# Optimization experiments

Measured on AMD Instinct MI355X. Metric: run time of the kernel, lower is better.

The kernel has to match this reference:

```python
import jax, jax.numpy as jnp
import numpy as np
from jax import lax

B, T, D, H, O = 64, 2048, 512, 512, 512


def setup_inputs() -> dict:
    key = jax.random.key(0)
    ks = jax.random.split(key, 8)
    s_in = 1.0 / np.sqrt(D)
    s_h = 1.0 / np.sqrt(H)
    s_o = 1.0 / np.sqrt(O)
    return {
        "embeddings": jax.random.normal(ks[0], (B, T, D), dtype=jnp.float32),
        "last_logits": jax.random.normal(ks[1], (B, O), dtype=jnp.float32),
        "Whx": jax.random.normal(ks[2], (H, D), dtype=jnp.float32) * s_in,
        "bhx": jax.random.normal(ks[3], (H,), dtype=jnp.float32) * s_in,
        "Wyh": jax.random.normal(ks[4], (H, O), dtype=jnp.float32) * s_o,
        "byh": jax.random.normal(ks[5], (H,), dtype=jnp.float32) * s_o,
        "Wout": jax.random.normal(ks[6], (O, H), dtype=jnp.float32) * s_h,
        "bout": jax.random.normal(ks[7], (O,), dtype=jnp.float32) * s_h,
    }


def reference(embeddings, last_logits, Whx, bhx, Wyh, byh, Wout, bout):
    # Precompute the input projection for all timesteps in one big GEMM:
    # xh[b,t,h] = hx(x_t)  (time-parallel part of the Jordan cell)
    xh = jnp.einsum('btd,hd->bth', embeddings, Whx) + bhx  # [B,T,H]

    def step(y_t, xh_t):
        # h_t = tanh(hx(x_t) + yh(y_t)); y_t = lm_head(h_t)
        h = jnp.tanh(xh_t + y_t @ Wyh.T + byh)   # [B,H]
        y = h @ Wout.T + bout                    # [B,O]
        return y, y

    last, ys = lax.scan(step, last_logits, jnp.swapaxes(xh, 0, 1))  # scan over T
    logits = jnp.swapaxes(ys, 0, 1)  # [B,T,O]
    return logits, last
```

## Files before the change

### kernel.cpp

```cpp
#include <hip/hip_runtime.h>
#include <hip/hip_bf16.h>


#define NB 64
#define NT 2048
#define ND 512
#define NH 512
#define NO 512
#define TH (NT * NH)

typedef float f32x4 __attribute__((ext_vector_type(4)));
typedef __bf16 bf16x8 __attribute__((ext_vector_type(8)));
typedef unsigned short u16x8 __attribute__((ext_vector_type(8)));

__device__ __forceinline__ unsigned short f2bf(float x) {
  unsigned u = __builtin_bit_cast(unsigned, x);
  u += 0x7FFFu + ((u >> 16) & 1u);
  return (unsigned short)(u >> 16);
}
__device__ __forceinline__ bf16x8 ld_frag(const unsigned short* p) {
  u16x8 r = *(const u16x8*)p;
  return __builtin_bit_cast(bf16x8, r);
}
__device__ __forceinline__ f32x4 ld_frag4(const unsigned short* p) {
  return *(const f32x4*)p;
}
__device__ __forceinline__ float fast_tanh(float x) {
  float ax = __builtin_fabsf(x);
  float e = __builtin_amdgcn_exp2f(ax * 2.8853900817779268f);
  float r = 1.0f - 2.0f * __builtin_amdgcn_rcpf(e + 1.0f);
  return __builtin_copysignf(r, x);
}


__global__ void k_bias(const float* __restrict__ Wyh, const float* __restrict__ bout,
                       const float* __restrict__ bhx, const float* __restrict__ byh,
                       float* bias_t0, float* bias_t) {
  int j = threadIdx.x;
  const float* row = Wyh + j * NO;
  float acc = 0.f;
  for (int o = 0; o < NO; ++o) acc += row[o] * bout[o];
  bias_t0[j] = bhx[j] + byh[j];
  bias_t[j]  = bhx[j] + byh[j] + acc;
}

__global__ void k_z0(const float* __restrict__ ll, const float* __restrict__ Wyh,
                     float* z0) {
  int b = blockIdx.x, j = threadIdx.x;
  const float* row = Wyh + j * NO;
  const float* lr = ll + b * NO;
  float acc = 0.f;
  for (int o = 0; o < NO; ++o) acc += lr[o] * row[o];
  z0[b * NH + j] = acc;
}

__global__ void k_wc(const float* __restrict__ Wyh, const float* __restrict__ Wout,
                     float* Wc) {
  int j = blockIdx.x, k = threadIdx.x;
  float acc = 0.f;
  for (int o = 0; o < NO; ++o) acc += Wyh[j * NO + o] * Wout[o * NH + k];
  Wc[j * NH + k] = acc;
}

__global__ void k_frag(const float* __restrict__ src, unsigned short* __restrict__ dst) {
  int gid = blockIdx.x * 256 + threadIdx.x;
  int lane = gid & 63, tidx = gid >> 6;
  int nt = tidx & 31, kt = tidx >> 5;
  const float* s = src + (size_t)(nt * 16 + (lane & 15)) * 512 + kt * 32 + (lane >> 4) * 8;
  unsigned short* d = dst + (size_t)gid * 8;
#pragma unroll
  for (int i = 0; i < 8; ++i) d[i] = f2bf(s[i]);
}

template <int MODE>
__global__ __launch_bounds__(512) void k_gemm(
    const void* __restrict__ Ain, const unsigned short* __restrict__ fragB,
    float* __restrict__ out, const float* __restrict__ bias_t0,
    const float* __restrict__ bias_t, const float* __restrict__ z0,
    const float* __restrict__ bout, float* __restrict__ last) {
  __shared__ __align__(16) unsigned short a_lds[64 * 512];
  int tid = threadIdx.x;
  long bt0 = (long)blockIdx.x * 64;

  if (MODE == 0) {
    const float* A = (const float*)Ain;
#pragma unroll
    for (int it = 0; it < 16; ++it) {
      int chunk = it * 512 + tid;
      int r = chunk >> 7, c4 = chunk & 127;
      float4 v = ((const float4*)A)[(bt0 + r) * 128 + c4];
      int idx = (r * 512 + c4 * 4) ^ ((r & 7) << 3);
      unsigned short* p = &a_lds[idx];
      p[0] = f2bf(v.x); p[1] = f2bf(v.y); p[2] = f2bf(v.z); p[3] = f2bf(v.w);
    }
  } else {
    const unsigned short* A = (const unsigned short*)Ain;
#pragma unroll
    for (int it = 0; it < 8; ++it) {
      int chunk = it * 512 + tid;
      int r = chunk >> 6, c8 = chunk & 63;
      u16x8 v = *(const u16x8*)(A + (size_t)(bt0 + r) * 1024 + c8 * 8);
      int idx = (r * 512 + c8 * 8) ^ ((r & 7) << 3);
      *(u16x8*)&a_lds[idx] = v;
    }
  }
  __syncthreads();

  int wave = tid >> 6, lane = tid & 63;
  int r0 = (wave & 3) * 16, c0 = (wave >> 2) * 256;
  f32x4 acc[16];
#pragma unroll
  for (int n = 0; n < 16; ++n) acc[n] = (f32x4){0.f, 0.f, 0.f, 0.f};
  int arow = r0 + (lane & 15);

  for (int kt = 0; kt < 16; ++kt) {
    int aidx = (arow * 512 + kt * 32 + (lane >> 4) * 8) ^ ((arow & 7) << 3);
    bf16x8 a = ld_frag(&a_lds[aidx]);
    const unsigned short* bp = fragB + ((size_t)(kt * 32 + (c0 >> 4)) * 64 + lane) * 8;
#pragma unroll
    for (int n = 0; n < 16; ++n) {
      bf16x8 b = ld_frag(bp + (size_t)n * 512);
      acc[n] = __builtin_amdgcn_mfma_f32_16x16x32_bf16(a, b, acc[n], 0, 0, 0);
    }
  }

#pragma unroll
  for (int n = 0; n < 16; ++n) {
    int col = c0 + n * 16 + (lane & 15);
#pragma unroll
    for (int reg = 0; reg < 4; ++reg) {
      long row = bt0 + r0 + (lane >> 4) * 4 + reg;
      float v = acc[n][reg];
      if (MODE == 0) {
        int t = (int)(row & (NT - 1));
        long b = row >> 11;
        v += (t == 0) ? (bias_t0[col] + z0[b * NH + col]) : bias_t[col];
      } else {
        v += bout[col];
      }
      out[row * 512 + col] = v;
      if (MODE == 1 && ((row & (NT - 1)) == NT - 1)) last[(row >> 11) * 512 + col] = v;
    }
  }
}

__global__ __launch_bounds__(512, 2) void k_scan(float* __restrict__ buf,
                                                 const unsigned short* __restrict__ fragWc) {
  __shared__ __align__(16) unsigned short h_lds[2][16 * 512];
  __shared__ __align__(16) unsigned short wc_lds[8 * 12 * 512];
  unsigned short* hbuf = (unsigned short*)buf;
  const int tid = threadIdx.x;
  const int b0 = blockIdx.x * 16;
  const int wave = tid >> 6, lane = tid & 63;
  const int arow = lane & 15, bb = lane >> 4;
  const int c0 = wave * 64;
  const int swz = (arow & 7) << 3;

  const unsigned short* bW = fragWc + ((size_t)(wave * 4) * 64 + lane) * 8;

#pragma unroll
  for (int g = 0; g < 3; ++g)
#pragma unroll
    for (int n = 0; n < 4; ++n) {
      f32x4 v = ld_frag4(bW + (size_t)((13 + g) * 32 + n) * 512);
      *(f32x4*)&wc_lds[(size_t)((wave * 3 + g) * 4 + n) * 512 + lane * 8] = v;
    }

  f32x4 br[7][4];
#pragma unroll
  for (int kt = 0; kt < 7; ++kt)
#pragma unroll
    for (int n = 0; n < 4; ++n) br[kt][n] = ld_frag4(bW + (size_t)(kt * 32 + n) * 512);
#pragma unroll
  for (int kt = 0; kt < 7; ++kt)
#pragma unroll
    for (int n = 0; n < 4; ++n) asm volatile("" : "+v"(br[kt][n]));

  float v0[16];
#pragma unroll
  for (int i = 0; i < 16; ++i) v0[i] = buf[(size_t)(b0 + i) * TH + tid];
  __syncthreads();
#pragma unroll
  for (int i = 0; i < 16; ++i) {
    float h = fast_tanh(v0[i]);
    unsigned short hb = f2bf(h);
    hbuf[(size_t)(b0 + i) * (size_t)NT * 1024 + tid] = hb;
    h_lds[0][(i * 512 + tid) ^ ((i & 7) << 3)] = hb;
  }

  const float* pPre[4];
  unsigned short* pSt[4];
#pragma unroll
  for (int r = 0; r < 4; ++r) {
    int b = b0 + bb * 4 + r;
    pPre[r] = buf + (size_t)b * TH + 512 + c0 + arow;
    pSt[r]  = hbuf + (size_t)b * (size_t)NT * 1024 + 1024 + c0 + arow;
  }

  float pre[16];
#pragma unroll
  for (int n = 0; n < 4; ++n)
#pragma unroll
    for (int r = 0; r < 4; ++r) pre[n * 4 + r] = pPre[r][n * 16];

  bf16x8 q0[4], q1[4], q2[4];
#pragma unroll
  for (int n = 0; n < 4; ++n) q0[n] = ld_frag(bW + (size_t)(7 * 32 + n) * 512);
#pragma unroll
  for (int n = 0; n < 4; ++n) q1[n] = ld_frag(bW + (size_t)(8 * 32 + n) * 512);
#pragma unroll
  for (int n = 0; n < 4; ++n) q2[n] = ld_frag(bW + (size_t)(9 * 32 + n) * 512);

  __syncthreads();

#define AIDX(k) ((arow * 512 + (k) * 32 + bb * 8) ^ swz)
#define STREAM_STEP(Q, KT, RKT)                                                     \
  {                                                                                 \
    bf16x8 a = ld_frag(hs + AIDX(KT));                                              \
    _Pragma("unroll") for (int n = 0; n < 4; ++n)                                   \
        acc[n] = __builtin_amdgcn_mfma_f32_16x16x32_bf16(a, Q[n], acc[n], 0, 0, 0); \
    _Pragma("unroll") for (int n = 0; n < 4; ++n)                                   \
        Q[n] = ld_frag(bWs + (size_t)((RKT) * 32 + n) * 512);                       \
  }

#pragma unroll 1
  for (int t = 1; t < NT; ++t) {
    const unsigned short* bWs = bW;
    asm volatile("" : "+v"(bWs));

    f32x4 acc[4];
#pragma unroll
    for (int n = 0; n < 4; ++n)
#pragma unroll
      for (int r = 0; r < 4; ++r) acc[n][r] = pre[n * 4 + r];

    const unsigned short* hs = h_lds[(t - 1) & 1];

#pragma unroll
    for (int kt = 0; kt < 7; ++kt) {
      bf16x8 a = ld_frag(hs + AIDX(kt));
#pragma unroll
      for (int n = 0; n < 4; ++n)
        acc[n] = __builtin_amdgcn_mfma_f32_16x16x32_bf16(
            a, __builtin_bit_cast(bf16x8, br[kt][n]), acc[n], 0, 0, 0);
    }

    STREAM_STEP(q0, 7, 10)
    STREAM_STEP(q1, 8, 11)
    STREAM_STEP(q2, 9, 12)
    STREAM_STEP(q0, 10, 7)
    STREAM_STEP(q1, 11, 8)
    STREAM_STEP(q2, 12, 9)

#pragma unroll
    for (int g = 0; g < 3; ++g) {
      bf16x8 a = ld_frag(hs + AIDX(13 + g));
#pragma unroll
      for (int n = 0; n < 4; ++n) {
        bf16x8 b = ld_frag(&wc_lds[(size_t)((wave * 3 + g) * 4 + n) * 512 + lane * 8]);
        acc[n] = __builtin_amdgcn_mfma_f32_16x16x32_bf16(a, b, acc[n], 0, 0, 0);
      }
    }

    if (t < NT - 1) {
#pragma unroll
      for (int r = 0; r < 4; ++r) pPre[r] += 512;
#pragma unroll
      for (int n = 0; n < 4; ++n)
#pragma unroll
        for (int r = 0; r < 4; ++r) pre[n * 4 + r] = pPre[r][n * 16];
    }

    unsigned short* hdst = h_lds[t & 1];
#pragma unroll
    for (int n = 0; n < 4; ++n)
#pragma unroll
      for (int r = 0; r < 4; ++r) {
        int b = bb * 4 + r;
        float h = fast_tanh(acc[n][r]);
        unsigned short hb = f2bf(h);
        pSt[r][n * 16] = hb;
        hdst[(b * 512 + c0 + n * 16 + arow) ^ ((b & 7) << 3)] = hb;
      }
#pragma unroll
    for (int r = 0; r < 4; ++r) pSt[r] += 1024;

    asm volatile("s_waitcnt lgkmcnt(0)" ::: "memory");
    __builtin_amdgcn_s_barrier();
    asm volatile("" ::: "memory");
  }
#undef STREAM_STEP
#undef AIDX
}

extern "C" void kernel_launch(void* const* d_in, const int* in_sizes, int n_in,
                              void* d_out, int out_size, void* d_ws, size_t ws_size,
                              hipStream_t stream) {
  const float* emb  = (const float*)d_in[0];
  const float* ll   = (const float*)d_in[1];
  const float* Whx  = (const float*)d_in[2];
  const float* bhx  = (const float*)d_in[3];
  const float* Wyh  = (const float*)d_in[4];
  const float* byh  = (const float*)d_in[5];
  const float* Wout = (const float*)d_in[6];
  const float* bout = (const float*)d_in[7];

  float* buf  = (float*)d_out;
  float* last = buf + (size_t)NB * NT * NO;

  char* ws = (char*)d_ws;
  unsigned short* fragWhx  = (unsigned short*)ws;
  unsigned short* fragWc   = (unsigned short*)(ws + (512 * 512 * 2));
  unsigned short* fragWout = (unsigned short*)(ws + 2 * (512 * 512 * 2));
  float* z0      = (float*)(ws + 3 * (512 * 512 * 2));
  float* bias_t0 = z0 + NB * NH;
  float* bias_t  = bias_t0 + NH;
  float* Wc_f32  = bias_t + NH;

  k_bias<<<1, 512, 0, stream>>>(Wyh, bout, bhx, byh, bias_t0, bias_t);
  k_z0<<<64, 512, 0, stream>>>(ll, Wyh, z0);
  k_wc<<<512, 512, 0, stream>>>(Wyh, Wout, Wc_f32);
  k_frag<<<128, 256, 0, stream>>>(Whx, fragWhx);
  k_frag<<<128, 256, 0, stream>>>(Wc_f32, fragWc);
  k_frag<<<128, 256, 0, stream>>>(Wout, fragWout);

  k_gemm<0><<<2048, 512, 0, stream>>>(emb, fragWhx, buf, bias_t0, bias_t, z0, bout, last);
  k_scan<<<4, 512, 0, stream>>>(buf, fragWc);
  k_gemm<1><<<2048, 512, 0, stream>>>(buf, fragWout, buf, bias_t0, bias_t, z0, bout, last);
}
```

Baseline: 8.362 ms.

## Store pre-activations as bf16 in scan-friendly layout and pin weights in AGPRs

```diff
diff --git a/kernel.cpp b/kernel.cpp
--- a/kernel.cpp
+++ b/kernel.cpp
@@ -12,11 +12,15 @@
 typedef float f32x4 __attribute__((ext_vector_type(4)));
 typedef __bf16 bf16x8 __attribute__((ext_vector_type(8)));
 typedef unsigned short u16x8 __attribute__((ext_vector_type(8)));
+typedef unsigned short u16x4 __attribute__((ext_vector_type(4)));
 
 __device__ __forceinline__ unsigned short f2bf(float x) {
   unsigned u = __builtin_bit_cast(unsigned, x);
   u += 0x7FFFu + ((u >> 16) & 1u);
   return (unsigned short)(u >> 16);
+}
+__device__ __forceinline__ float bf2f(unsigned short u) {
+  return __builtin_bit_cast(float, (unsigned)u << 16);
 }
 __device__ __forceinline__ bf16x8 ld_frag(const unsigned short* p) {
   u16x8 r = *(const u16x8*)p;
@@ -72,6 +76,11 @@
   for (int i = 0; i < 8; ++i) d[i] = f2bf(s[i]);
 }
 
+__device__ __forceinline__ int pre_idx(int col) {
+  int w = col >> 7;
+  return w * 128 + ((w >> 1) << 9) + (col & 15) * 8 + ((col >> 4) & 7);
+}
+
 template <int MODE>
 __global__ __launch_bounds__(512) void k_gemm(
     const void* __restrict__ Ain, const unsigned short* __restrict__ fragB,
@@ -99,7 +108,7 @@
     for (int it = 0; it < 8; ++it) {
       int chunk = it * 512 + tid;
       int r = chunk >> 6, c8 = chunk & 63;
-      u16x8 v = *(const u16x8*)(A + (size_t)(bt0 + r) * 1024 + c8 * 8);
+      u16x8 v = *(const u16x8*)(A + (size_t)(bt0 + r) * 1024 + 256 + c8 * 8);
       int idx = (r * 512 + c8 * 8) ^ ((r & 7) << 3);
       *(u16x8*)&a_lds[idx] = v;
     }
@@ -135,11 +144,12 @@
         int t = (int)(row & (NT - 1));
         long b = row >> 11;
         v += (t == 0) ? (bias_t0[col] + z0[b * NH + col]) : bias_t[col];
+        ((unsigned short*)out)[row * 1024 + pre_idx(col)] = f2bf(v);
       } else {
         v += bout[col];
+        out[row * 512 + col] = v;
+        if ((row & (NT - 1)) == NT - 1) last[(row >> 11) * 512 + col] = v;
       }
-      out[row * 512 + col] = v;
-      if (MODE == 1 && ((row & (NT - 1)) == NT - 1)) last[(row >> 11) * 512 + col] = v;
     }
   }
 }
@@ -155,6 +165,8 @@
   const int arow = lane & 15, bb = lane >> 4;
   const int c0 = wave * 64;
   const int swz = (arow & 7) << 3;
+  const int w2 = wave >> 1;
+  const int poff = w2 * 128 + ((w2 >> 1) << 9) + arow * 8 + (wave & 1) * 4;
 
   const unsigned short* bW = fragWc + ((size_t)(wave * 4) * 64 + lane) * 8;
 
@@ -166,61 +178,73 @@
       *(f32x4*)&wc_lds[(size_t)((wave * 3 + g) * 4 + n) * 512 + lane * 8] = v;
     }
 
-  f32x4 br[7][4];
-#pragma unroll
-  for (int kt = 0; kt < 7; ++kt)
-#pragma unroll
-    for (int n = 0; n < 4; ++n) br[kt][n] = ld_frag4(bW + (size_t)(kt * 32 + n) * 512);
-#pragma unroll
-  for (int kt = 0; kt < 7; ++kt)
-#pragma unroll
-    for (int n = 0; n < 4; ++n) asm volatile("" : "+v"(br[kt][n]));
-
-  float v0[16];
-#pragma unroll
-  for (int i = 0; i < 16; ++i) v0[i] = buf[(size_t)(b0 + i) * TH + tid];
+  f32x4 ba[9][4];
+#pragma unroll
+  for (int g = 0; g < 9; ++g)
+#pragma unroll
+    for (int n = 0; n < 4; ++n) ba[g][n] = ld_frag4(bW + (size_t)(g * 32 + n) * 512);
+#pragma unroll
+  for (int g = 0; g < 9; ++g)
+#pragma unroll
+    for (int n = 0; n < 4; ++n) asm volatile("" : "+a"(ba[g][n]));
+
+  u16x4 pr[4];
+#pragma unroll
+  for (int r = 0; r < 4; ++r)
+    pr[r] = *(const u16x4*)(hbuf + (size_t)(b0 + bb * 4 + r) * (size_t)(NT * 1024) + poff);
+#pragma unroll
+  for (int r = 0; r < 4; ++r)
+#pragma unroll
+    for (int n = 0; n < 4; ++n) {
+      float h = fast_tanh(bf2f(pr[r][n]));
+      unsigned short hb = f2bf(h);
+      int b = bb * 4 + r, col = c0 + n * 16 + arow;
+      hbuf[(size_t)(b0 + b) * (size_t)(NT * 1024) + 256 + col] = hb;
+      h_lds[0][(b * 512 + col) ^ ((b & 7) << 3)] = hb;
+    }
+
+  const unsigned short* pPre[4];
+  unsigned short* pSt[4];
+#pragma unroll
+  for (int r = 0; r < 4; ++r) {
+    size_t base = (size_t)(b0 + bb * 4 + r) * (size_t)(NT * 1024) + 1024;
+    pPre[r] = hbuf + base + poff;
+    pSt[r]  = hbuf + base + 256 + c0 + arow;
+  }
+#pragma unroll
+  for (int r = 0; r < 4; ++r) pr[r] = *(const u16x4*)pPre[r];
+
+  bf16x8 q0[4], q1[4];
+#pragma unroll
+  for (int n = 0; n < 4; ++n) q0[n] = ld_frag(bW + (size_t)(9 * 32 + n) * 512);
+#pragma unroll
+  for (int n = 0; n < 4; ++n) q1[n] = ld_frag(bW + (size_t)(10 * 32 + n) * 512);
+
   __syncthreads();
-#pragma unroll
-  for (int i = 0; i < 16; ++i) {
-    float h = fast_tanh(v0[i]);
-    unsigned short hb = f2bf(h);
-    hbuf[(size_t)(b0 + i) * (size_t)NT * 1024 + tid] = hb;
-    h_lds[0][(i * 512 + tid) ^ ((i & 7) << 3)] = hb;
-  }
-
-  const float* pPre[4];
-  unsigned short* pSt[4];
-#pragma unroll
-  for (int r = 0; r < 4; ++r) {
-    int b = b0 + bb * 4 + r;
-    pPre[r] = buf + (size_t)b * TH + 512 + c0 + arow;
-    pSt[r]  = hbuf + (size_t)b * (size_t)NT * 1024 + 1024 + c0 + arow;
-  }
-
-  float pre[16];
-#pragma unroll
-  for (int n = 0; n < 4; ++n)
-#pragma unroll
-    for (int r = 0; r < 4; ++r) pre[n * 4 + r] = pPre[r][n * 16];
-
-  bf16x8 q0[4], q1[4], q2[4];
-#pragma unroll
-  for (int n = 0; n < 4; ++n) q0[n] = ld_frag(bW + (size_t)(7 * 32 + n) * 512);
-#pragma unroll
-  for (int n = 0; n < 4; ++n) q1[n] = ld_frag(bW + (size_t)(8 * 32 + n) * 512);
-#pragma unroll
-  for (int n = 0; n < 4; ++n) q2[n] = ld_frag(bW + (size_t)(9 * 32 + n) * 512);
-
-  __syncthreads();
 
 #define AIDX(k) ((arow * 512 + (k) * 32 + bb * 8) ^ swz)
-#define STREAM_STEP(Q, KT, RKT)                                                     \
-  {                                                                                 \
-    bf16x8 a = ld_frag(hs + AIDX(KT));                                              \
-    _Pragma("unroll") for (int n = 0; n < 4; ++n)                                   \
+#define AGPR_STEP(G)                                                            \
+  {                                                                             \
+    bf16x8 a = ld_frag(hs + AIDX(G));                                           \
+    _Pragma("unroll") for (int n = 0; n < 4; ++n)                               \
+        acc[n] = __builtin_amdgcn_mfma_f32_16x16x32_bf16(                       \
+            a, __builtin_bit_cast(bf16x8, ba[G][n]), acc[n], 0, 0, 0);          \
+  }
+#define STREAM_STEP(Q, KT, RKT)                                                 \
+  {                                                                             \
+    bf16x8 a = ld_frag(hs + AIDX(KT));                                          \
+    _Pragma("unroll") for (int n = 0; n < 4; ++n)                               \
         acc[n] = __builtin_amdgcn_mfma_f32_16x16x32_bf16(a, Q[n], acc[n], 0, 0, 0); \
-    _Pragma("unroll") for (int n = 0; n < 4; ++n)                                   \
-        Q[n] = ld_frag(bWs + (size_t)((RKT) * 32 + n) * 512);                       \
+    _Pragma("unroll") for (int n = 0; n < 4; ++n)                               \
+        Q[n] = ld_frag(bWs + (size_t)((RKT) * 32 + n) * 512);                   \
+  }
+#define LDS_STEP(G)                                                             \
+  {                                                                             \
+    bf16x8 a = ld_frag(hs + AIDX(13 + G));                                      \
+    _Pragma("unroll") for (int n = 0; n < 4; ++n) {                             \
+      bf16x8 b = ld_frag(&wc_lds[(size_t)((wave * 3 + (G)) * 4 + n) * 512 + lane * 8]); \
+      acc[n] = __builtin_amdgcn_mfma_f32_16x16x32_bf16(a, b, acc[n], 0, 0, 0);  \
+    }                                                                           \
   }
 
 #pragma unroll 1
@@ -232,43 +256,27 @@
 #pragma unroll
     for (int n = 0; n < 4; ++n)
 #pragma unroll
-      for (int r = 0; r < 4; ++r) acc[n][r] = pre[n * 4 + r];
+      for (int r = 0; r < 4; ++r) acc[n][r] = bf2f(pr[r][n]);
 
     const unsigned short* hs = h_lds[(t - 1) & 1];
 
-#pragma unroll
-    for (int kt = 0; kt < 7; ++kt) {
-      bf16x8 a = ld_frag(hs + AIDX(kt));
-#pragma unroll
-      for (int n = 0; n < 4; ++n)
-        acc[n] = __builtin_amdgcn_mfma_f32_16x16x32_bf16(
-            a, __builtin_bit_cast(bf16x8, br[kt][n]), acc[n], 0, 0, 0);
-    }
-
-    STREAM_STEP(q0, 7, 10)
-    STREAM_STEP(q1, 8, 11)
-    STREAM_STEP(q2, 9, 12)
-    STREAM_STEP(q0, 10, 7)
-    STREAM_STEP(q1, 11, 8)
-    STREAM_STEP(q2, 12, 9)
-
-#pragma unroll
-    for (int g = 0; g < 3; ++g) {
-      bf16x8 a = ld_frag(hs + AIDX(13 + g));
-#pragma unroll
-      for (int n = 0; n < 4; ++n) {
-        bf16x8 b = ld_frag(&wc_lds[(size_t)((wave * 3 + g) * 4 + n) * 512 + lane * 8]);
-        acc[n] = __builtin_amdgcn_mfma_f32_16x16x32_bf16(a, b, acc[n], 0, 0, 0);
+    AGPR_STEP(0) AGPR_STEP(1) AGPR_STEP(2) AGPR_STEP(3)
+    STREAM_STEP(q0, 9, 11)
+    AGPR_STEP(4) AGPR_STEP(5) AGPR_STEP(6) AGPR_STEP(7)
+    STREAM_STEP(q1, 10, 12)
+    AGPR_STEP(8)
+    LDS_STEP(0)
+    STREAM_STEP(q0, 11, 9)
+    LDS_STEP(1)
+    STREAM_STEP(q1, 12, 10)
+    LDS_STEP(2)
+
+    if (t < NT - 1) {
+#pragma unroll
+      for (int r = 0; r < 4; ++r) {
+        pPre[r] += 1024;
+        pr[r] = *(const u16x4*)pPre[r];
       }
-    }
-
-    if (t < NT - 1) {
-#pragma unroll
-      for (int r = 0; r < 4; ++r) pPre[r] += 512;
-#pragma unroll
-      for (int n = 0; n < 4; ++n)
-#pragma unroll
-        for (int r = 0; r < 4; ++r) pre[n * 4 + r] = pPre[r][n * 16];
     }
 
     unsigned short* hdst = h_lds[t & 1];
@@ -289,7 +297,9 @@
     __builtin_amdgcn_s_barrier();
     asm volatile("" ::: "memory");
   }
+#undef LDS_STEP
 #undef STREAM_STEP
+#undef AGPR_STEP
 #undef AIDX
 }
 
```

After: 7.774 ms. 1.08x faster.
